# Kernel tuning notes

Measured on AMD Instinct MI355X. Metric: run time of the kernel, lower is better.

## Reference

```python
import jax, jax.numpy as jnp
import numpy as np

NTYPES = 2
NATOMS = (512, 512)
N = 1024          # total atoms
NN = 128          # neighbors per type
M = NTYPES * NN   # 256 neighbor slots per atom
D = 25            # last embedding width
FH = 240          # fitting hidden width
B = 8
RMIN, RMAX = 5.8, 6.0


def _embed_mlp(s, W0, b0, W1, b1, W2, b2):
    # DeepMD-style resnet embedding net: 1 -> D -> D -> D, tanh + skip
    h = jnp.tanh(s @ W0 + b0)
    h = h + jnp.tanh(h @ W1 + b1)
    h = h + jnp.tanh(h @ W2 + b2)
    return h


def setup_inputs() -> dict:
    key = jax.random.key(0)
    ks = jax.random.split(key, 20)
    # relative positions; components in [-4.5, 4.5] so |r| spans <5.8, [5.8,6.0), >=6.0
    image_dR = (jax.random.uniform(ks[0], (B, N, NTYPES, NN, 3), jnp.float32) - 0.5) * 9.0
    # 0 == empty neighbor slot (mask = list_neigh > 0); index-1 in [0, N)
    list_neigh = jax.random.randint(ks[1], (B, N, NTYPES, NN), 0, 1025)
    davg = 0.1 * jax.random.normal(ks[2], (NTYPES, M, 4), jnp.float32)
    dstd = jax.random.uniform(ks[3], (NTYPES, M, 4), jnp.float32, 0.5, 1.5)
    P = NTYPES * NTYPES
    eW0 = jax.random.normal(ks[4], (P, 1, D), jnp.float32)
    eb0 = 0.1 * jax.random.normal(ks[5], (P, D), jnp.float32)
    eW1 = jax.random.normal(ks[6], (P, D, D), jnp.float32) / np.sqrt(D)
    eb1 = 0.1 * jax.random.normal(ks[7], (P, D), jnp.float32)
    eW2 = jax.random.normal(ks[8], (P, D, D), jnp.float32) / np.sqrt(D)
    eb2 = 0.1 * jax.random.normal(ks[9], (P, D), jnp.float32)
    fW0 = jax.random.normal(ks[10], (NTYPES, 16 * D, FH), jnp.float32) / np.sqrt(16 * D)
    fb0 = 0.1 * jax.random.normal(ks[11], (NTYPES, FH), jnp.float32)
    fW1 = jax.random.normal(ks[12], (NTYPES, FH, FH), jnp.float32) / np.sqrt(FH)
    fb1 = 0.1 * jax.random.normal(ks[13], (NTYPES, FH), jnp.float32)
    fW2 = jax.random.normal(ks[14], (NTYPES, FH, FH), jnp.float32) / np.sqrt(FH)
    fb2 = 0.1 * jax.random.normal(ks[15], (NTYPES, FH), jnp.float32)
    fW3 = jax.random.normal(ks[16], (NTYPES, FH, 1), jnp.float32) / np.sqrt(FH)
    fb3 = 0.1 * jax.random.normal(ks[17], (NTYPES, 1), jnp.float32)
    ener_shift = 0.01 * jax.random.normal(ks[18], (NTYPES,), jnp.float32)
    return {
        'image_dR': image_dR, 'list_neigh': list_neigh,
        'davg': davg, 'dstd': dstd,
        'eW0': eW0, 'eb0': eb0, 'eW1': eW1, 'eb1': eb1, 'eW2': eW2, 'eb2': eb2,
        'fW0': fW0, 'fb0': fb0, 'fW1': fW1, 'fb1': fb1, 'fW2': fW2, 'fb2': fb2,
        'fW3': fW3, 'fb3': fb3, 'ener_shift': ener_shift,
        'dfeat': jnp.zeros((1,), jnp.float32),
        'Egroup_weight': jnp.zeros((1,), jnp.float32),
        'divider': jnp.ones((1,), jnp.float32),
    }


def _forward(image_dR, list_neigh, davg, dstd,
             eW0, eb0, eW1, eb1, eW2, eb2,
             fW0, fb0, fW1, fb1, fW2, fb2, fW3, fb3, ener_shift):
    dR = image_dR.reshape(B, N, M, 3)
    neigh = list_neigh.reshape(B, N, M)
    mask = neigh > 0
    mf = mask.astype(dR.dtype)
    dR2 = jnp.sum(dR * dR, axis=-1)                       # [B,N,M]
    safe_dR2 = jnp.where(mask, dR2, 1.0)
    Rij = jnp.sqrt(safe_dR2)
    inr = mf / Rij                                        # 1/|r|, 0 off-mask
    x = Rij * mf                                          # nr = dR2/Rij = |r|
    Ri_xyz = dR / safe_dR2[..., None] * mf[..., None]     # r / |r|^2
    inr2 = inr * inr
    inr4 = inr2 * inr2
    inr3 = inr4 * x
    # smooth switching function on [RMIN, RMAX]
    u = (x - RMIN) / (RMAX - RMIN)
    poly = u * u * u * (-6.0 * u * u + 15.0 * u - 10.0) + 1.0
    dpoly = (3.0 * u * u * (-6.0 * u * u + 15.0 * u - 10.0)
             + u * u * u * (-12.0 * u + 15.0)) / (RMAX - RMIN)
    mid = (x >= RMIN) & (x < RMAX)
    vv = jnp.where(x < RMIN, 1.0, jnp.where(mid, poly, 0.0)) * mf
    dvv = jnp.where(mid, dpoly, 0.0) * mf
    Ri_pre = jnp.concatenate([inr[..., None], Ri_xyz], axis=-1)   # [B,N,M,4]
    common = (dvv * inr)[..., None] * dR                          # [B,N,M,3]
    row0 = dR * (inr3 * vv)[..., None] - Ri_pre[..., 0:1] * common
    eye = jnp.eye(3, dtype=dR.dtype)
    outer = (2.0 * dR[..., :, None] * dR[..., None, :] * inr4[..., None, None]
             - eye * inr2[..., None, None])                       # [B,N,M,3,3]
    rows = outer * vv[..., None, None] - Ri_pre[..., 1:4, None] * common[..., None, :]
    Ri_d = jnp.concatenate([row0[..., None, :], rows], axis=-2) * mf[..., None, None]  # [B,N,M,4,3]
    Ri = Ri_pre * vv[..., None]
    # per-type normalization stats broadcast over atoms of each type
    davg_res = jnp.concatenate([jnp.broadcast_to(davg[t], (NATOMS[t], M, 4)) for t in range(NTYPES)], axis=0)
    dstd_res = jnp.concatenate([jnp.broadcast_to(dstd[t], (NATOMS[t], M, 4)) for t in range(NTYPES)], axis=0)
    Ri = (Ri - davg_res) / dstd_res
    Ri_d = Ri_d / dstd_res[..., None]

    def ei_fn(Ri_n):
        Ei_list = []
        start = 0
        for t in range(NTYPES):
            na = NATOMS[t]
            Rt = jax.lax.slice_in_dim(Ri_n, start, start + na, axis=1)  # [B,na,M,4]
            acc = jnp.zeros((B, na, 4, D), Ri_n.dtype)
            for t1 in range(NTYPES):
                p = t * NTYPES + t1
                blk = Rt[:, :, t1 * NN:(t1 + 1) * NN]                  # [B,na,NN,4]
                G = _embed_mlp(blk[..., 0:1], eW0[p], eb0[p], eW1[p], eb1[p], eW2[p], eb2[p])
                acc = acc + jnp.einsum('bnkd,bnke->bnde', blk, G)
            acc = acc * (4.0 / (NN * NTYPES * 4))
            DRt = jnp.einsum('bnde,bndf->bnef', acc, acc[..., :16]).reshape(B, na, D * 16)
            h = jnp.tanh(DRt @ fW0[t] + fb0[t])
            h = h + jnp.tanh(h @ fW1[t] + fb1[t])
            h = h + jnp.tanh(h @ fW2[t] + fb2[t])
            Ei_list.append(h @ fW3[t] + fb3[t] + ener_shift[t])
            start += na
        return jnp.concatenate(Ei_list, axis=1)   # [B,N,1]

    Ei, vjpf = jax.vjp(ei_fn, Ri)
    dE, = vjpf(jnp.ones_like(Ei))                 # dEi/dRi  [B,N,M,4]
    Etot = jnp.sum(Ei, axis=1)                    # [B,1]
    pair = jnp.einsum('bnmd,bnmdx->bnmx', dE, Ri_d)   # per-pair force term [B,N,M,3]
    F_self = -jnp.sum(pair, axis=2)
    j = neigh - 1
    valid = j >= 0
    flat_idx = jnp.where(valid, j, N) + jnp.arange(B)[:, None, None] * (N + 1)
    contrib = jnp.where(valid[..., None], pair, 0.0)
    seg = jax.ops.segment_sum(contrib.reshape(-1, 3), flat_idx.reshape(-1), num_segments=B * (N + 1))
    F = F_self + seg.reshape(B, N + 1, 3)[:, :N]
    return Etot, Ei, F


def reference(image_dR, list_neigh, davg, dstd,
              eW0, eb0, eW1, eb1, eW2, eb2,
              fW0, fb0, fW1, fb1, fW2, fb2, fW3, fb3, ener_shift,
              dfeat, Egroup_weight, divider):
    # dfeat / Egroup_weight / divider are in the torch forward signature but unused
    return _forward(image_dR, list_neigh, davg, dstd,
                    eW0, eb0, eW1, eb1, eW2, eb2,
                    fW0, fb0, fW1, fb1, fW2, fb2, fW3, fb3, ener_shift)
```

## Files before the change

kernel.cpp:

```cpp
#include <hip/hip_runtime.h>

#define DEV __device__ __forceinline__

namespace {

constexpr int B_ = 8;
constexpr int N_ = 1024;
constexpr int M_ = 256;
constexpr int D_ = 25;
constexpr int FH_ = 240;
constexpr int NATOM = B_ * N_;
constexpr float CSC = 1.0f / 256.0f;

DEV float fast_tanh(float x) {
  float ax = fabsf(x);
  float e = __expf(-2.0f * ax);
  float r = (1.0f - e) * __builtin_amdgcn_rcpf(1.0f + e);
  return copysignf(r, x);
}

template <bool WANT_RID>
DEV void compute_geom(float dx, float dy, float dz, int nb, int t, int m,
                      const float* __restrict__ davg, const float* __restrict__ dstd,
                      float* __restrict__ blk, float* __restrict__ rid) {
  float mf = (nb > 0) ? 1.0f : 0.0f;
  float dr2 = dx * dx + dy * dy + dz * dz;
  float safe = (nb > 0) ? dr2 : 1.0f;
  float rs = __builtin_amdgcn_rsqf(safe);
  float rij = safe * rs;
  float inr = mf * rs;
  float x = rij * mf;
  float inr2 = inr * inr;
  float inr4 = inr2 * inr2;
  float inr3 = inr4 * x;
  float u = (x - 5.8f) * 5.0f;
  float uu = u * u;
  float A = -6.0f * uu + 15.0f * u - 10.0f;
  float poly = uu * u * A + 1.0f;
  float dpoly = (3.0f * uu * A + uu * u * (-12.0f * u + 15.0f)) * 5.0f;
  bool mid = (x >= 5.8f) && (x < 6.0f);
  float vv = ((x < 5.8f) ? 1.0f : (mid ? poly : 0.0f)) * mf;
  float dvv = (mid ? dpoly : 0.0f) * mf;
  float pre[4];
  pre[0] = inr;
  pre[1] = dx * inr2;
  pre[2] = dy * inr2;
  pre[3] = dz * inr2;
  int bidx = (t * M_ + m) * 4;
  float4 av = *(const float4*)(davg + bidx);
  float4 sv = *(const float4*)(dstd + bidx);
  float avf[4] = {av.x, av.y, av.z, av.w};
  float rsv[4] = {__builtin_amdgcn_rcpf(sv.x), __builtin_amdgcn_rcpf(sv.y),
                  __builtin_amdgcn_rcpf(sv.z), __builtin_amdgcn_rcpf(sv.w)};
#pragma unroll
  for (int d = 0; d < 4; ++d) blk[d] = (pre[d] * vv - avf[d]) * rsv[d];
  if (WANT_RID) {
    float dv[3] = {dx, dy, dz};
    float ci = dvv * inr;
    float com[3];
#pragma unroll
    for (int c = 0; c < 3; ++c) com[c] = ci * dv[c];
    float iv = inr3 * vv;
#pragma unroll
    for (int c = 0; c < 3; ++c)
      rid[c] = (dv[c] * iv - pre[0] * com[c]) * mf * rsv[0];
#pragma unroll
    for (int r = 0; r < 3; ++r) {
#pragma unroll
      for (int c = 0; c < 3; ++c) {
        float outer = 2.0f * dv[r] * dv[c] * inr4 - ((r == c) ? inr2 : 0.0f);
        rid[(1 + r) * 3 + c] = (outer * vv - pre[1 + r] * com[c]) * mf * rsv[1 + r];
      }
    }
  }
}

DEV void embed_fwd(float s, const float* __restrict__ W0, const float* __restrict__ b0,
                   const float* __restrict__ W1, const float* __restrict__ b1,
                   const float* __restrict__ W2, const float* __restrict__ b2,
                   float* __restrict__ h0, float* __restrict__ t1v,
                   float* __restrict__ h1, float* __restrict__ t2v) {
#pragma unroll
  for (int e = 0; e < D_; ++e) h0[e] = fast_tanh(fmaf(s, W0[e], b0[e]));
  float a[D_];
#pragma unroll
  for (int e = 0; e < D_; ++e) a[e] = b1[e];
#pragma unroll
  for (int f = 0; f < D_; ++f) {
    float hf = h0[f];
#pragma unroll
    for (int e = 0; e < D_; ++e) a[e] = fmaf(hf, W1[f * D_ + e], a[e]);
  }
#pragma unroll
  for (int e = 0; e < D_; ++e) { t1v[e] = fast_tanh(a[e]); h1[e] = h0[e] + t1v[e]; }
#pragma unroll
  for (int e = 0; e < D_; ++e) a[e] = b2[e];
#pragma unroll
  for (int f = 0; f < D_; ++f) {
    float hf = h1[f];
#pragma unroll
    for (int e = 0; e < D_; ++e) a[e] = fmaf(hf, W2[f * D_ + e], a[e]);
  }
#pragma unroll
  for (int e = 0; e < D_; ++e) t2v[e] = fast_tanh(a[e]);
}

__global__ __launch_bounds__(256, 2) void k_embed_acc(
    const float* __restrict__ dR, const int* __restrict__ neigh,
    const float* __restrict__ davg, const float* __restrict__ dstd,
    const float* __restrict__ eW0, const float* __restrict__ eb0,
    const float* __restrict__ eW1, const float* __restrict__ eb1,
    const float* __restrict__ eW2, const float* __restrict__ eb2,
    float* __restrict__ acc_ws) {
  __shared__ float sG[M_ * D_];
  __shared__ float4 sBlk[M_];
  int atom = blockIdx.x;
  int n = atom & (N_ - 1);
  int t = (n >= 512) ? 1 : 0;
  int m = threadIdx.x;
  int p = __builtin_amdgcn_readfirstlane(t * 2 + (m >> 7));
  const float* W0 = eW0 + p * D_;
  const float* b0 = eb0 + p * D_;
  const float* W1 = eW1 + p * D_ * D_;
  const float* b1 = eb1 + p * D_;
  const float* W2 = eW2 + p * D_ * D_;
  const float* b2 = eb2 + p * D_;
  int base = atom * M_ + m;
  float dx = dR[base * 3 + 0];
  float dy = dR[base * 3 + 1];
  float dz = dR[base * 3 + 2];
  int nb = neigh[base];
  float blk[4];
  compute_geom<false>(dx, dy, dz, nb, t, m, davg, dstd, blk, nullptr);
  float h0[D_], t1v[D_], h1[D_], t2v[D_];
  embed_fwd(blk[0], W0, b0, W1, b1, W2, b2, h0, t1v, h1, t2v);
#pragma unroll
  for (int e = 0; e < D_; ++e) sG[m * D_ + e] = h1[e] + t2v[e];
  sBlk[m] = make_float4(blk[0], blk[1], blk[2], blk[3]);
  __syncthreads();
  if (threadIdx.x < 100) {
    int d = threadIdx.x & 3;
    int e = threadIdx.x >> 2;
    const float* sb = (const float*)sBlk;
    float sum = 0.0f;
    for (int mm = 0; mm < M_; ++mm)
      sum = fmaf(sb[mm * 4 + d], sG[mm * D_ + e], sum);
    acc_ws[atom * 100 + d * D_ + e] = sum * CSC;
  }
}

__global__ __launch_bounds__(256) void k_fit(
    const float* __restrict__ acc_ws,
    const float* __restrict__ fW0, const float* __restrict__ fb0,
    const float* __restrict__ fW1, const float* __restrict__ fb1,
    const float* __restrict__ fW2, const float* __restrict__ fb2,
    const float* __restrict__ fW3, const float* __restrict__ fb3,
    const float* __restrict__ ener_shift,
    float* __restrict__ dacc_ws, float* __restrict__ out) {
  constexpr int AB = 8;
  __shared__ float sAcc[AB][100];
  __shared__ float sX[AB][400];
  __shared__ float sH0[AB][FH_];
  __shared__ float sT1[AB][FH_];
  __shared__ float sH1[AB][FH_];
  __shared__ float sT2[AB][FH_];
  __shared__ float sEi[AB];
  int a0 = blockIdx.x * AB;
  int bb = a0 >> 10;
  int n0 = a0 & (N_ - 1);
  int t = (n0 >= 512) ? 1 : 0;
  int tid = threadIdx.x;
  for (int idx = tid; idx < AB * 100; idx += 256)
    ((float*)sAcc)[idx] = acc_ws[a0 * 100 + idx];
  if (tid < AB) sEi[tid] = 0.0f;
  __syncthreads();
  for (int idx = tid; idx < AB * 400; idx += 256) {
    int a = idx / 400; int r = idx % 400; int e = r >> 4; int f = r & 15;
    const float* A = sAcc[a];
    sX[a][r] = A[e] * A[f] + A[25 + e] * A[25 + f] + A[50 + e] * A[50 + f] +
               A[75 + e] * A[75 + f];
  }
  __syncthreads();
  const float* W0 = fW0 + t * 400 * FH_;
  const float* W1 = fW1 + t * FH_ * FH_;
  const float* W2 = fW2 + t * FH_ * FH_;
  const float* B0 = fb0 + t * FH_;
  const float* B1 = fb1 + t * FH_;
  const float* B2 = fb2 + t * FH_;
  const float* W3 = fW3 + t * FH_;
  int j = tid;
  if (j < FH_) {
    float acc8[AB];
#pragma unroll
    for (int a = 0; a < AB; ++a) acc8[a] = B0[j];
    for (int i = 0; i < 400; ++i) {
      float w = W0[i * FH_ + j];
#pragma unroll
      for (int a = 0; a < AB; ++a) acc8[a] = fmaf(sX[a][i], w, acc8[a]);
    }
#pragma unroll
    for (int a = 0; a < AB; ++a) sH0[a][j] = fast_tanh(acc8[a]);
  }
  __syncthreads();
  if (j < FH_) {
    float acc8[AB];
#pragma unroll
    for (int a = 0; a < AB; ++a) acc8[a] = B1[j];
    for (int f = 0; f < FH_; ++f) {
      float w = W1[f * FH_ + j];
#pragma unroll
      for (int a = 0; a < AB; ++a) acc8[a] = fmaf(sH0[a][f], w, acc8[a]);
    }
#pragma unroll
    for (int a = 0; a < AB; ++a) {
      float tv = fast_tanh(acc8[a]);
      sT1[a][j] = tv;
      sH1[a][j] = sH0[a][j] + tv;
    }
  }
  __syncthreads();
  if (j < FH_) {
    float acc8[AB];
#pragma unroll
    for (int a = 0; a < AB; ++a) acc8[a] = B2[j];
    for (int f = 0; f < FH_; ++f) {
      float w = W2[f * FH_ + j];
#pragma unroll
      for (int a = 0; a < AB; ++a) acc8[a] = fmaf(sH1[a][f], w, acc8[a]);
    }
    float w3 = W3[j];
#pragma unroll
    for (int a = 0; a < AB; ++a) {
      float tv = fast_tanh(acc8[a]);
      sT2[a][j] = tv;
      atomicAdd(&sEi[a], (sH1[a][j] + tv) * w3);
    }
  }
  __syncthreads();
  if (tid < AB) {
    float ei = sEi[tid] + fb3[t] + ener_shift[t];
    out[8 + a0 + tid] = ei;
    atomicAdd(&out[bb], ei);
  }
  if (j < FH_) {
    float w3 = W3[j];
#pragma unroll
    for (int a = 0; a < AB; ++a) {
      float tv = sT2[a][j];
      sT2[a][j] = w3 * (1.0f - tv * tv);
    }
  }
  __syncthreads();
  if (j < FH_) {
    float w3 = W3[j];
    float acc8[AB];
#pragma unroll
    for (int a = 0; a < AB; ++a) acc8[a] = w3;
    for (int k = 0; k < FH_; ++k) {
      float w = W2[j * FH_ + k];
#pragma unroll
      for (int a = 0; a < AB; ++a) acc8[a] = fmaf(sT2[a][k], w, acc8[a]);
    }
#pragma unroll
    for (int a = 0; a < AB; ++a) {
      float dh1 = acc8[a];
      float tv = sT1[a][j];
      sH1[a][j] = dh1;
      sT1[a][j] = dh1 * (1.0f - tv * tv);
    }
  }
  __syncthreads();
  if (j < FH_) {
    float acc8[AB];
#pragma unroll
    for (int a = 0; a < AB; ++a) acc8[a] = sH1[a][j];
    for (int k = 0; k < FH_; ++k) {
      float w = W1[j * FH_ + k];
#pragma unroll
      for (int a = 0; a < AB; ++a) acc8[a] = fmaf(sT1[a][k], w, acc8[a]);
    }
#pragma unroll
    for (int a = 0; a < AB; ++a) {
      float h0v = sH0[a][j];
      sH0[a][j] = acc8[a] * (1.0f - h0v * h0v);
    }
  }
  __syncthreads();
  for (int i = tid; i < 400; i += 256) {
    float acc8[AB];
#pragma unroll
    for (int a = 0; a < AB; ++a) acc8[a] = 0.0f;
    for (int jj = 0; jj < FH_; ++jj) {
      float w = W0[i * FH_ + jj];
#pragma unroll
      for (int a = 0; a < AB; ++a) acc8[a] = fmaf(sH0[a][jj], w, acc8[a]);
    }
#pragma unroll
    for (int a = 0; a < AB; ++a) sX[a][i] = acc8[a];
  }
  __syncthreads();
  for (int idx = tid; idx < AB * 100; idx += 256) {
    int a = idx / 100; int r = idx % 100; int d = r / 25; int e = r % 25;
    const float* A = sAcc[a];
    const float* DX = sX[a];
    float sum = 0.0f;
#pragma unroll
    for (int f = 0; f < 16; ++f) sum = fmaf(DX[e * 16 + f], A[d * 25 + f], sum);
    if (e < 16) {
#pragma unroll
      for (int e2 = 0; e2 < 25; ++e2) sum = fmaf(DX[e2 * 16 + e], A[d * 25 + e2], sum);
    }
    dacc_ws[a0 * 100 + idx] = sum;
  }
}

__global__ __launch_bounds__(256, 2) void k_bwd_force(
    const float* __restrict__ dR, const int* __restrict__ neigh,
    const float* __restrict__ davg, const float* __restrict__ dstd,
    const float* __restrict__ eW0, const float* __restrict__ eb0,
    const float* __restrict__ eW1, const float* __restrict__ eb1,
    const float* __restrict__ eW2, const float* __restrict__ eb2,
    const float* __restrict__ dacc_ws, float* __restrict__ out) {
  __shared__ float sF[3];
  int atom = blockIdx.x;
  int bb = atom >> 10;
  int n = atom & (N_ - 1);
  int t = (n >= 512) ? 1 : 0;
  int m = threadIdx.x;
  if (m < 3) sF[m] = 0.0f;
  __syncthreads();
  int p = __builtin_amdgcn_readfirstlane(t * 2 + (m >> 7));
  const float* W0 = eW0 + p * D_;
  const float* b0 = eb0 + p * D_;
  const float* W1 = eW1 + p * D_ * D_;
  const float* b1 = eb1 + p * D_;
  const float* W2 = eW2 + p * D_ * D_;
  const float* b2 = eb2 + p * D_;
  const float* dac = dacc_ws + atom * 100;
  int base = atom * M_ + m;
  float dx = dR[base * 3 + 0];
  float dy = dR[base * 3 + 1];
  float dz = dR[base * 3 + 2];
  int nb = neigh[base];
  float blk[4], rid[12];
  compute_geom<true>(dx, dy, dz, nb, t, m, davg, dstd, blk, rid);
  float h0[D_], t1v[D_], h1[D_], t2v[D_];
  embed_fwd(blk[0], W0, b0, W1, b1, W2, b2, h0, t1v, h1, t2v);
  float dblk[4];
#pragma unroll
  for (int d = 0; d < 4; ++d) {
    float s = 0.0f;
#pragma unroll
    for (int e = 0; e < D_; ++e) s = fmaf(dac[d * D_ + e], h1[e] + t2v[e], s);
    dblk[d] = s * CSC;
  }
  float dG[D_];
#pragma unroll
  for (int e = 0; e < D_; ++e)
    dG[e] = CSC * (dac[e] * blk[0] + dac[25 + e] * blk[1] +
                   dac[50 + e] * blk[2] + dac[75 + e] * blk[3]);
  float g[D_];
#pragma unroll
  for (int e = 0; e < D_; ++e) g[e] = dG[e] * (1.0f - t2v[e] * t2v[e]);
#pragma unroll
  for (int e = 0; e < D_; ++e) {
    float s = dG[e];
#pragma unroll
    for (int f = 0; f < D_; ++f) s = fmaf(g[f], W2[e * D_ + f], s);
    dG[e] = s;
  }
#pragma unroll
  for (int e = 0; e < D_; ++e) g[e] = dG[e] * (1.0f - t1v[e] * t1v[e]);
#pragma unroll
  for (int e = 0; e < D_; ++e) {
    float s = dG[e];
#pragma unroll
    for (int f = 0; f < D_; ++f) s = fmaf(g[f], W1[e * D_ + f], s);
    dG[e] = s;
  }
  float ds = 0.0f;
#pragma unroll
  for (int e = 0; e < D_; ++e) ds = fmaf(dG[e] * (1.0f - h0[e] * h0[e]), W0[e], ds);
  float dE0 = dblk[0] + ds, dE1 = dblk[1], dE2 = dblk[2], dE3 = dblk[3];
  float px = dE0 * rid[0] + dE1 * rid[3] + dE2 * rid[6] + dE3 * rid[9];
  float py = dE0 * rid[1] + dE1 * rid[4] + dE2 * rid[7] + dE3 * rid[10];
  float pz = dE0 * rid[2] + dE1 * rid[5] + dE2 * rid[8] + dE3 * rid[11];
  atomicAdd(&sF[0], px);
  atomicAdd(&sF[1], py);
  atomicAdd(&sF[2], pz);
  if (nb > 0) {
    int jn = nb - 1;
    int fi = 8 + NATOM + (bb * N_ + jn) * 3;
    atomicAdd(&out[fi + 0], px);
    atomicAdd(&out[fi + 1], py);
    atomicAdd(&out[fi + 2], pz);
  }
  __syncthreads();
  if (m < 3) atomicAdd(&out[8 + NATOM + atom * 3 + m], -sF[m]);
}

}

extern "C" void kernel_launch(void* const* d_in, const int* in_sizes, int n_in,
                              void* d_out, int out_size, void* d_ws, size_t ws_size,
                              hipStream_t stream) {
  (void)in_sizes; (void)n_in; (void)ws_size;
  const float* image_dR   = (const float*)d_in[0];
  const int*   list_neigh = (const int*)d_in[1];
  const float* davg       = (const float*)d_in[2];
  const float* dstd       = (const float*)d_in[3];
  const float* eW0        = (const float*)d_in[4];
  const float* eb0        = (const float*)d_in[5];
  const float* eW1        = (const float*)d_in[6];
  const float* eb1        = (const float*)d_in[7];
  const float* eW2        = (const float*)d_in[8];
  const float* eb2        = (const float*)d_in[9];
  const float* fW0        = (const float*)d_in[10];
  const float* fb0        = (const float*)d_in[11];
  const float* fW1        = (const float*)d_in[12];
  const float* fb1        = (const float*)d_in[13];
  const float* fW2        = (const float*)d_in[14];
  const float* fb2        = (const float*)d_in[15];
  const float* fW3        = (const float*)d_in[16];
  const float* fb3        = (const float*)d_in[17];
  const float* ener_shift = (const float*)d_in[18];
  float* out = (float*)d_out;
  float* acc_ws  = (float*)d_ws;
  float* dacc_ws = acc_ws + NATOM * 100;

  hipMemsetAsync(d_out, 0, (size_t)out_size * sizeof(float), stream);
  k_embed_acc<<<NATOM, 256, 0, stream>>>(image_dR, list_neigh, davg, dstd,
                                         eW0, eb0, eW1, eb1, eW2, eb2, acc_ws);
  k_fit<<<NATOM / 8, 256, 0, stream>>>(acc_ws, fW0, fb0, fW1, fb1, fW2, fb2,
                                       fW3, fb3, ener_shift, dacc_ws, out);
  k_bwd_force<<<NATOM, 256, 0, stream>>>(image_dR, list_neigh, davg, dstd,
                                         eW0, eb0, eW1, eb1, eW2, eb2,
                                         dacc_ws, out);
}
```

Before: 1.054 ms.

## Cut register pressure in embed kernels and privatize neighbor force scatter

Inlines the embedding forward with in-place reuse of arrays to lower register pressure. The backward kernel now spills h0/t1 activations to transposed shared memory and computes the geometry derivative late, both to shorten live ranges. Neighbor force atomics are spread over 16 partial buffers and summed by a new reduce kernel, which avoids contention on global atomics. The embed contraction uses a transposed, float4 shared layout, and per-block energy sums are merged into a single atomic. Costs are an extra memset of about 1.5 MB, an extra kernel launch, and more shared memory per block.

```diff
diff --git a/kernel.cpp b/kernel.cpp
--- a/kernel.cpp
+++ b/kernel.cpp
@@ -10,7 +10,14 @@
 constexpr int D_ = 25;
 constexpr int FH_ = 240;
 constexpr int NATOM = B_ * N_;
+constexpr int NPART = 16;
 constexpr float CSC = 1.0f / 256.0f;
+
+constexpr int ACC_OFF  = 0;
+constexpr int DACC_OFF = NATOM * 100;
+constexpr int SELF_OFF = DACC_OFF + NATOM * 100;
+constexpr int FPART_OFF = SELF_OFF + NATOM * 3;
+constexpr int WS_FLOATS = FPART_OFF + NPART * NATOM * 3;
 
 DEV float fast_tanh(float x) {
   float ax = fabsf(x);
@@ -75,36 +82,6 @@
   }
 }
 
-DEV void embed_fwd(float s, const float* __restrict__ W0, const float* __restrict__ b0,
-                   const float* __restrict__ W1, const float* __restrict__ b1,
-                   const float* __restrict__ W2, const float* __restrict__ b2,
-                   float* __restrict__ h0, float* __restrict__ t1v,
-                   float* __restrict__ h1, float* __restrict__ t2v) {
-#pragma unroll
-  for (int e = 0; e < D_; ++e) h0[e] = fast_tanh(fmaf(s, W0[e], b0[e]));
-  float a[D_];
-#pragma unroll
-  for (int e = 0; e < D_; ++e) a[e] = b1[e];
-#pragma unroll
-  for (int f = 0; f < D_; ++f) {
-    float hf = h0[f];
-#pragma unroll
-    for (int e = 0; e < D_; ++e) a[e] = fmaf(hf, W1[f * D_ + e], a[e]);
-  }
-#pragma unroll
-  for (int e = 0; e < D_; ++e) { t1v[e] = fast_tanh(a[e]); h1[e] = h0[e] + t1v[e]; }
-#pragma unroll
-  for (int e = 0; e < D_; ++e) a[e] = b2[e];
-#pragma unroll
-  for (int f = 0; f < D_; ++f) {
-    float hf = h1[f];
-#pragma unroll
-    for (int e = 0; e < D_; ++e) a[e] = fmaf(hf, W2[f * D_ + e], a[e]);
-  }
-#pragma unroll
-  for (int e = 0; e < D_; ++e) t2v[e] = fast_tanh(a[e]);
-}
-
 __global__ __launch_bounds__(256, 2) void k_embed_acc(
     const float* __restrict__ dR, const int* __restrict__ neigh,
     const float* __restrict__ davg, const float* __restrict__ dstd,
@@ -112,8 +89,8 @@
     const float* __restrict__ eW1, const float* __restrict__ eb1,
     const float* __restrict__ eW2, const float* __restrict__ eb2,
     float* __restrict__ acc_ws) {
-  __shared__ float sG[M_ * D_];
-  __shared__ float4 sBlk[M_];
+  __shared__ float sGT[D_][260];
+  __shared__ float sBT[4][260];
   int atom = blockIdx.x;
   int n = atom & (N_ - 1);
   int t = (n >= 512) ? 1 : 0;
@@ -132,19 +109,44 @@
   int nb = neigh[base];
   float blk[4];
   compute_geom<false>(dx, dy, dz, nb, t, m, davg, dstd, blk, nullptr);
-  float h0[D_], t1v[D_], h1[D_], t2v[D_];
-  embed_fwd(blk[0], W0, b0, W1, b1, W2, b2, h0, t1v, h1, t2v);
-#pragma unroll
-  for (int e = 0; e < D_; ++e) sG[m * D_ + e] = h1[e] + t2v[e];
-  sBlk[m] = make_float4(blk[0], blk[1], blk[2], blk[3]);
+  float s0 = blk[0];
+  float H[D_], a[D_];
+#pragma unroll
+  for (int e = 0; e < D_; ++e) H[e] = fast_tanh(fmaf(s0, W0[e], b0[e]));
+#pragma unroll
+  for (int e = 0; e < D_; ++e) a[e] = b1[e];
+#pragma unroll
+  for (int f = 0; f < D_; ++f) {
+    float hf = H[f];
+#pragma unroll
+    for (int e = 0; e < D_; ++e) a[e] = fmaf(hf, W1[f * D_ + e], a[e]);
+  }
+#pragma unroll
+  for (int e = 0; e < D_; ++e) H[e] += fast_tanh(a[e]);
+#pragma unroll
+  for (int e = 0; e < D_; ++e) a[e] = b2[e];
+#pragma unroll
+  for (int f = 0; f < D_; ++f) {
+    float hf = H[f];
+#pragma unroll
+    for (int e = 0; e < D_; ++e) a[e] = fmaf(hf, W2[f * D_ + e], a[e]);
+  }
+#pragma unroll
+  for (int e = 0; e < D_; ++e) sGT[e][m] = H[e] + fast_tanh(a[e]);
+#pragma unroll
+  for (int d = 0; d < 4; ++d) sBT[d][m] = blk[d];
   __syncthreads();
   if (threadIdx.x < 100) {
+    int e = threadIdx.x >> 2;
     int d = threadIdx.x & 3;
-    int e = threadIdx.x >> 2;
-    const float* sb = (const float*)sBlk;
+    const float4* g4 = (const float4*)(&sGT[e][0]);
+    const float4* b4 = (const float4*)(&sBT[d][0]);
     float sum = 0.0f;
-    for (int mm = 0; mm < M_; ++mm)
-      sum = fmaf(sb[mm * 4 + d], sG[mm * D_ + e], sum);
+    for (int k = 0; k < 64; ++k) {
+      float4 g = g4[k];
+      float4 b = b4[k];
+      sum += b.x * g.x + b.y * g.y + b.z * g.z + b.w * g.w;
+    }
     acc_ws[atom * 100 + d * D_ + e] = sum * CSC;
   }
 }
@@ -240,7 +242,7 @@
   if (tid < AB) {
     float ei = sEi[tid] + fb3[t] + ener_shift[t];
     out[8 + a0 + tid] = ei;
-    atomicAdd(&out[bb], ei);
+    sEi[tid] = ei;
   }
   if (j < FH_) {
     float w3 = W3[j];
@@ -251,6 +253,10 @@
     }
   }
   __syncthreads();
+  if (tid == 0) {
+    float s = sEi[0] + sEi[1] + sEi[2] + sEi[3] + sEi[4] + sEi[5] + sEi[6] + sEi[7];
+    atomicAdd(&out[bb], s);
+  }
   if (j < FH_) {
     float w3 = W3[j];
     float acc8[AB];
@@ -320,7 +326,10 @@
     const float* __restrict__ eW0, const float* __restrict__ eb0,
     const float* __restrict__ eW1, const float* __restrict__ eb1,
     const float* __restrict__ eW2, const float* __restrict__ eb2,
-    const float* __restrict__ dacc_ws, float* __restrict__ out) {
+    const float* __restrict__ dacc_ws, float* __restrict__ self_ws,
+    float* __restrict__ fpart) {
+  __shared__ float sH0[D_][M_];
+  __shared__ float sT1[D_][M_];
   __shared__ float sF[3];
   int atom = blockIdx.x;
   int bb = atom >> 10;
@@ -342,46 +351,79 @@
   float dy = dR[base * 3 + 1];
   float dz = dR[base * 3 + 2];
   int nb = neigh[base];
-  float blk[4], rid[12];
-  compute_geom<true>(dx, dy, dz, nb, t, m, davg, dstd, blk, rid);
-  float h0[D_], t1v[D_], h1[D_], t2v[D_];
-  embed_fwd(blk[0], W0, b0, W1, b1, W2, b2, h0, t1v, h1, t2v);
-  float dblk[4];
-#pragma unroll
-  for (int d = 0; d < 4; ++d) {
-    float s = 0.0f;
-#pragma unroll
-    for (int e = 0; e < D_; ++e) s = fmaf(dac[d * D_ + e], h1[e] + t2v[e], s);
-    dblk[d] = s * CSC;
-  }
-  float dG[D_];
-#pragma unroll
-  for (int e = 0; e < D_; ++e)
-    dG[e] = CSC * (dac[e] * blk[0] + dac[25 + e] * blk[1] +
-                   dac[50 + e] * blk[2] + dac[75 + e] * blk[3]);
-  float g[D_];
-#pragma unroll
-  for (int e = 0; e < D_; ++e) g[e] = dG[e] * (1.0f - t2v[e] * t2v[e]);
-#pragma unroll
-  for (int e = 0; e < D_; ++e) {
-    float s = dG[e];
-#pragma unroll
-    for (int f = 0; f < D_; ++f) s = fmaf(g[f], W2[e * D_ + f], s);
-    dG[e] = s;
-  }
-#pragma unroll
-  for (int e = 0; e < D_; ++e) g[e] = dG[e] * (1.0f - t1v[e] * t1v[e]);
-#pragma unroll
-  for (int e = 0; e < D_; ++e) {
-    float s = dG[e];
-#pragma unroll
-    for (int f = 0; f < D_; ++f) s = fmaf(g[f], W1[e * D_ + f], s);
-    dG[e] = s;
-  }
-  float ds = 0.0f;
-#pragma unroll
-  for (int e = 0; e < D_; ++e) ds = fmaf(dG[e] * (1.0f - h0[e] * h0[e]), W0[e], ds);
-  float dE0 = dblk[0] + ds, dE1 = dblk[1], dE2 = dblk[2], dE3 = dblk[3];
+  float blk[4];
+  compute_geom<false>(dx, dy, dz, nb, t, m, davg, dstd, blk, nullptr);
+  float s0 = blk[0];
+  float X[D_], Y[D_];
+#pragma unroll
+  for (int e = 0; e < D_; ++e) {
+    float h = fast_tanh(fmaf(s0, W0[e], b0[e]));
+    X[e] = h;
+    sH0[e][m] = h;
+  }
+#pragma unroll
+  for (int e = 0; e < D_; ++e) Y[e] = b1[e];
+#pragma unroll
+  for (int f = 0; f < D_; ++f) {
+    float hf = X[f];
+#pragma unroll
+    for (int e = 0; e < D_; ++e) Y[e] = fmaf(hf, W1[f * D_ + e], Y[e]);
+  }
+#pragma unroll
+  for (int e = 0; e < D_; ++e) {
+    float tv = fast_tanh(Y[e]);
+    sT1[e][m] = tv;
+    X[e] += tv;
+  }
+#pragma unroll
+  for (int e = 0; e < D_; ++e) Y[e] = b2[e];
+#pragma unroll
+  for (int f = 0; f < D_; ++f) {
+    float hf = X[f];
+#pragma unroll
+    for (int e = 0; e < D_; ++e) Y[e] = fmaf(hf, W2[f * D_ + e], Y[e]);
+  }
+  float dblk0 = 0.0f, dblk1 = 0.0f, dblk2 = 0.0f, dblk3 = 0.0f;
+#pragma unroll
+  for (int e = 0; e < D_; ++e) {
+    float t2 = fast_tanh(Y[e]);
+    float G = X[e] + t2;
+    dblk0 = fmaf(dac[e], G, dblk0);
+    dblk1 = fmaf(dac[25 + e], G, dblk1);
+    dblk2 = fmaf(dac[50 + e], G, dblk2);
+    dblk3 = fmaf(dac[75 + e], G, dblk3);
+    float dGe = CSC * (dac[e] * blk[0] + dac[25 + e] * blk[1] +
+                       dac[50 + e] * blk[2] + dac[75 + e] * blk[3]);
+    Y[e] = dGe * (1.0f - t2 * t2);
+    X[e] = dGe;
+  }
+#pragma unroll
+  for (int e = 0; e < D_; ++e) {
+    float s = X[e];
+#pragma unroll
+    for (int f = 0; f < D_; ++f) s = fmaf(Y[f], W2[e * D_ + f], s);
+    X[e] = s;
+  }
+#pragma unroll
+  for (int e = 0; e < D_; ++e) {
+    float tv = sT1[e][m];
+    Y[e] = X[e] * (1.0f - tv * tv);
+  }
+  float dsum = 0.0f;
+#pragma unroll
+  for (int e = 0; e < D_; ++e) {
+    float s = X[e];
+#pragma unroll
+    for (int f = 0; f < D_; ++f) s = fmaf(Y[f], W1[e * D_ + f], s);
+    float h0e = sH0[e][m];
+    dsum = fmaf(s * (1.0f - h0e * h0e), W0[e], dsum);
+  }
+  float dE0 = dblk0 * CSC + dsum;
+  float dE1 = dblk1 * CSC;
+  float dE2 = dblk2 * CSC;
+  float dE3 = dblk3 * CSC;
+  float blk2b[4], rid[12];
+  compute_geom<true>(dx, dy, dz, nb, t, m, davg, dstd, blk2b, rid);
   float px = dE0 * rid[0] + dE1 * rid[3] + dE2 * rid[6] + dE3 * rid[9];
   float py = dE0 * rid[1] + dE1 * rid[4] + dE2 * rid[7] + dE3 * rid[10];
   float pz = dE0 * rid[2] + dE1 * rid[5] + dE2 * rid[8] + dE3 * rid[11];
@@ -390,13 +432,25 @@
   atomicAdd(&sF[2], pz);
   if (nb > 0) {
     int jn = nb - 1;
-    int fi = 8 + NATOM + (bb * N_ + jn) * 3;
-    atomicAdd(&out[fi + 0], px);
-    atomicAdd(&out[fi + 1], py);
-    atomicAdd(&out[fi + 2], pz);
-  }
-  __syncthreads();
-  if (m < 3) atomicAdd(&out[8 + NATOM + atom * 3 + m], -sF[m]);
+    float* fp = fpart + (atom & (NPART - 1)) * (NATOM * 3) + (bb * N_ + jn) * 3;
+    atomicAdd(fp + 0, px);
+    atomicAdd(fp + 1, py);
+    atomicAdd(fp + 2, pz);
+  }
+  __syncthreads();
+  if (m < 3) self_ws[atom * 3 + m] = sF[m];
+}
+
+__global__ __launch_bounds__(256) void k_force_reduce(
+    const float* __restrict__ self_ws, const float* __restrict__ fpart,
+    float* __restrict__ out) {
+  int idx = blockIdx.x * 256 + threadIdx.x;
+  if (idx < NATOM * 3) {
+    float s = -self_ws[idx];
+#pragma unroll
+    for (int k = 0; k < NPART; ++k) s += fpart[k * (NATOM * 3) + idx];
+    out[8 + NATOM + idx] = s;
+  }
 }
 
 }
@@ -425,15 +479,21 @@
   const float* fb3        = (const float*)d_in[17];
   const float* ener_shift = (const float*)d_in[18];
   float* out = (float*)d_out;
-  float* acc_ws  = (float*)d_ws;
-  float* dacc_ws = acc_ws + NATOM * 100;
+  float* ws = (float*)d_ws;
+  float* acc_ws  = ws + ACC_OFF;
+  float* dacc_ws = ws + DACC_OFF;
+  float* self_ws = ws + SELF_OFF;
+  float* fpart   = ws + FPART_OFF;
 
   hipMemsetAsync(d_out, 0, (size_t)out_size * sizeof(float), stream);
+  hipMemsetAsync(ws + SELF_OFF, 0,
+                 (size_t)(WS_FLOATS - SELF_OFF) * sizeof(float), stream);
   k_embed_acc<<<NATOM, 256, 0, stream>>>(image_dR, list_neigh, davg, dstd,
                                          eW0, eb0, eW1, eb1, eW2, eb2, acc_ws);
   k_fit<<<NATOM / 8, 256, 0, stream>>>(acc_ws, fW0, fb0, fW1, fb1, fW2, fb2,
                                        fW3, fb3, ener_shift, dacc_ws, out);
   k_bwd_force<<<NATOM, 256, 0, stream>>>(image_dR, list_neigh, davg, dstd,
                                          eW0, eb0, eW1, eb1, eW2, eb2,
-                                         dacc_ws, out);
-}
+                                         dacc_ws, self_ws, fpart);
+  k_force_reduce<<<(NATOM * 3 + 255) / 256, 256, 0, stream>>>(self_ws, fpart, out);
+}
```

Result: slower. 1.092 ms (+3.7%).
